# Kernel optimization log

Hardware: AMD Instinct MI355X
Metric: run time of the kernel (lower is better)

Reference implementation:

```python
import jax, jax.numpy as jnp
import numpy as np

B, S, H = 2, 4096, 768
E, R, D = 2, 4, 256          # engines, state_rank, prod(state_mode_sizes)=16*16
FEAT = 6 + 2 * R              # engine_state_feature_dim
IMPRESSION_RATE = 0.05
EPS = 1e-6


def setup_inputs() -> dict:
    key = jax.random.key(0)
    ks = jax.random.split(key, 20)
    n = jax.random.normal
    inv = lambda f: 1.0 / np.sqrt(f)
    return {
        "x": n(ks[0], (B, S, H), jnp.float32),
        # ComplexLinear signal_proj: hidden -> state_dim
        "Wsig_r": n(ks[1], (H, D), jnp.float32) * inv(H),
        "Wsig_i": n(ks[2], (H, D), jnp.float32) * inv(H),
        "bsig_r": jnp.zeros((D,), jnp.float32),
        "bsig_i": jnp.zeros((D,), jnp.float32),
        # per-engine complex recurrence params [E,R,D]
        "log_decay": n(ks[3], (E, R, D), jnp.float32) * 0.5 + 2.0,
        "theta": n(ks[4], (E, R, D), jnp.float32) * 0.1,
        "Bin_r": n(ks[5], (E, R, D), jnp.float32) * inv(D),
        "Bin_i": n(ks[6], (E, R, D), jnp.float32) * inv(D),
        # per-engine ComplexLinear feat -> hidden  [E,FEAT,H]
        "Wsh_r": n(ks[7], (E, FEAT, H), jnp.float32) * inv(FEAT),
        "Wsh_i": n(ks[8], (E, FEAT, H), jnp.float32) * inv(FEAT),
        "bsh_r": jnp.zeros((E, H), jnp.float32),
        "bsh_i": jnp.zeros((E, H), jnp.float32),
        # fusion ComplexLinear: hidden*E -> hidden
        "Wfus_r": n(ks[9], (E * H, H), jnp.float32) * inv(E * H),
        "Wfus_i": n(ks[10], (E * H, H), jnp.float32) * inv(E * H),
        "bfus_r": jnp.zeros((H,), jnp.float32),
        "bfus_i": jnp.zeros((H,), jnp.float32),
        # gate: Linear(hidden*4 -> hidden)
        "Wgate": n(ks[11], (4 * H, H), jnp.float32) * inv(4 * H),
        "bgate": jnp.zeros((H,), jnp.float32),
    }


def _mixer(x, Wsig_r, Wsig_i, bsig_r, bsig_i, log_decay, theta, Bin_r, Bin_i,
           Wsh_r, Wsh_i, bsh_r, bsh_i, Wfus_r, Wfus_i, bfus_r, bfus_i, Wgate, bgate):
    b, s, _ = x.shape
    # complex signal projection (input is real): [b,s,D]
    sr = x @ Wsig_r + bsig_r
    si = x @ Wsig_i + bsig_i
    # input term per engine/rank: u = B * signal  -> [b,s,E,R,D]
    sre = sr[:, :, None, None, :]
    sie = si[:, :, None, None, :]
    ur = Bin_r * sre - Bin_i * sie
    ui = Bin_r * sie + Bin_i * sre
    # complex decay lambda = exp(-softplus(log_decay)) * exp(i*theta)
    mag = jnp.exp(-jax.nn.softplus(log_decay))
    lr = mag * jnp.cos(theta)
    li = mag * jnp.sin(theta)
    ar = jnp.broadcast_to(lr, ur.shape)
    ai = jnp.broadcast_to(li, ur.shape)

    def comb(c1, c2):
        a1r, a1i, b1r, b1i = c1
        a2r, a2i, b2r, b2i = c2
        return (a1r * a2r - a1i * a2i,
                a1r * a2i + a1i * a2r,
                a2r * b1r - a2i * b1i + b2r,
                a2r * b1i + a2i * b1r + b2i)

    # parallel prefix scan of the linear recurrence h_t = lam*h_{t-1} + u_t (time axis=1)
    _, _, hr, hi = jax.lax.associative_scan(comb, (ar, ai, ur, ui), axis=1)

    # rmsnorm over mode dim of complex magnitude
    inv = jax.lax.rsqrt(jnp.mean(hr * hr + hi * hi, axis=-1, keepdims=True) + EPS)
    hr = hr * inv
    hi = hi * inv
    # nonlinear reciprocation-style correction
    hr2 = hr * (1.0 + IMPRESSION_RATE * jnp.tanh(hi))
    hi2 = hi * (1.0 + IMPRESSION_RATE * jnp.tanh(hr))
    hr, hi = hr2, hi2

    # engine state features: FEAT = 6 + 2R complex scalars per (b,s,e)
    f1r, f1i = hr.mean(-1), hi.mean(-1)                        # [b,s,E,R]
    f2r = (hr * hr - hi * hi).mean(-1)
    f2i = (2.0 * hr * hi).mean(-1)
    p = hr * hr + hi * hi
    g1r, g1i = hr.mean((-2, -1)), hi.mean((-2, -1))            # [b,s,E]
    g2r = (hr * hr - hi * hi).mean((-2, -1))
    g2i = (2.0 * hr * hi).mean((-2, -1))
    g3r = p.mean((-2, -1)); g3i = jnp.zeros_like(g3r)
    g4r = jnp.tanh(hr).mean((-2, -1)); g4i = jnp.tanh(hi).mean((-2, -1))
    g5r = jnp.sqrt((hr * hr).mean((-2, -1)) + EPS)
    g5i = jnp.sqrt((hi * hi).mean((-2, -1)) + EPS)
    g6r = (hr * hi).mean((-2, -1)); g6i = jnp.zeros_like(g6r)
    gr = jnp.stack([g1r, g2r, g3r, g4r, g5r, g6r], axis=-1)    # [b,s,E,6]
    gi = jnp.stack([g1i, g2i, g3i, g4i, g5i, g6i], axis=-1)
    fr = jnp.concatenate([f1r, f2r, gr], axis=-1)              # [b,s,E,FEAT]
    fi = jnp.concatenate([f1i, f2i, gi], axis=-1)

    # per-engine complex projection feat -> hidden
    yr = jnp.einsum('bsef,efh->bseh', fr, Wsh_r) - jnp.einsum('bsef,efh->bseh', fi, Wsh_i) + bsh_r
    yi = jnp.einsum('bsef,efh->bseh', fr, Wsh_i) + jnp.einsum('bsef,efh->bseh', fi, Wsh_r) + bsh_i
    yrf = yr.reshape(b, s, -1)
    yif = yi.reshape(b, s, -1)
    # engine fusion ComplexLinear (hidden*E -> hidden)
    fur = yrf @ Wfus_r - yif @ Wfus_i + bfus_r
    fui = yrf @ Wfus_i + yif @ Wfus_r + bfus_i
    # gated residual output
    gate_in = jnp.concatenate([x, fur, fui, fur * jax.nn.silu(fui)], axis=-1)
    gate = jax.nn.sigmoid(gate_in @ Wgate + bgate)
    return x + gate * fur


def reference(x, Wsig_r, Wsig_i, bsig_r, bsig_i, log_decay, theta, Bin_r, Bin_i,
              Wsh_r, Wsh_i, bsh_r, bsh_i, Wfus_r, Wfus_i, bfus_r, bfus_i, Wgate, bgate):
    return _mixer(x, Wsig_r, Wsig_i, bsig_r, bsig_i, log_decay, theta, Bin_r, Bin_i,
                  Wsh_r, Wsh_i, bsh_r, bsh_i, Wfus_r, Wfus_i, bfus_r, bfus_i, Wgate, bgate)
```

## Files before the change

### kernel.cpp

```cpp
#include <hip/hip_runtime.h>
#include <cstdint>
#include <cstddef>

#define B_ 2
#define S_ 4096
#define H_ 768
#define E_ 2
#define R_ 4
#define D_ 256
#define M_ (B_*S_)
#define NC_ 512
#define LC_ (S_/NC_)
#define KGATE 3072
#define KC_ 16
#define HCHUNK (H_/KC_)
#define NF_ 15

typedef __attribute__((ext_vector_type(4))) float f32x4;
typedef __attribute__((ext_vector_type(8))) short short8;

#define GLL(gsrc, ldst) \
  __builtin_amdgcn_global_load_lds((const __attribute__((address_space(1))) void*)(gsrc), \
                                   (__attribute__((address_space(3))) void*)(ldst), 16, 0, 0)

__device__ __forceinline__ unsigned short f2b(float f){
  union { float f; unsigned u; } v; v.f = f;
  unsigned u = v.u;
  return (unsigned short)((u + 0x7fffu + ((u >> 16) & 1u)) >> 16);
}
__device__ __forceinline__ float b2f(unsigned short b){
  union { unsigned u; float f; } v; v.u = ((unsigned)b) << 16;
  return v.f;
}

__device__ __forceinline__ float ftanh(float x){
  float e = __expf(2.f*x);
  return 1.f - 2.f*__builtin_amdgcn_rcpf(e + 1.f);
}
__device__ __forceinline__ float fsigmoid(float x){
  return __builtin_amdgcn_rcpf(1.f + __expf(-x));
}

__device__ __forceinline__ int permK(int r){
  if (r < 768)  return r;
  if (r < 1536) return 768 + 2*(r - 768);
  if (r < 2304) return 769 + 2*(r - 1536);
  return r;
}

__global__ __launch_bounds__(256) void prep_k(
    const float* __restrict__ x, unsigned short* __restrict__ Agate,
    const float* __restrict__ Wsig_r, const float* __restrict__ Wsig_i,
    const float* __restrict__ Wgate,
    unsigned short* __restrict__ WsigT, unsigned short* __restrict__ WgateT,
    const float* __restrict__ Wsh_r, const float* __restrict__ Wsh_i,
    const float* __restrict__ bsh_r, const float* __restrict__ bsh_i,
    const float* __restrict__ Wfus_r, const float* __restrict__ Wfus_i,
    float* __restrict__ Pr, float* __restrict__ Pi)
{
  __shared__ __align__(16) float smem[1440];
  const int bid = blockIdx.x;
  const int tid = threadIdx.x;

  if (bid < 6144){
    int t = bid*256 + tid;
    int base = t*4;
    int m = base / H_, h = base % H_;
    float4 v = *(const float4*)(x + base);
    ushort4 o;
    o.x = f2b(v.x); o.y = f2b(v.y); o.z = f2b(v.z); o.w = f2b(v.w);
    *(ushort4*)(Agate + (size_t)m*KGATE + h) = o;
    return;
  }
  if (bid < 13056){
    int idx = bid - 6144;
    int z = idx / 2304;
    int rem = idx % 2304;
    int bx = rem % 24, by = rem / 24;
    float (*tile)[33] = (float(*)[33])smem;
    const float* in_; unsigned short* out_; int Rr, Cc;
    if (z == 2){ in_ = Wgate; out_ = WgateT; Rr = 3072; Cc = 768; }
    else { in_ = z ? Wsig_i : Wsig_r; out_ = WsigT + (size_t)z*256*768; Rr = 768; Cc = 256; }
    int c0 = bx*32, r0 = by*32;
    if (c0 >= Cc || r0 >= Rr) return;
    int tx = tid & 31, ty = tid >> 5;
    for (int i = ty; i < 32; i += 8){
      int r = r0 + i, c = c0 + tx;
      tile[i][tx] = (r < Rr && c < Cc) ? in_[(size_t)r*Cc + c] : 0.f;
    }
    __syncthreads();
    for (int i = ty; i < 32; i += 8){
      int c = c0 + i, r = r0 + tx;
      if (c < Cc && r < Rr){
        int rd = (z == 2) ? permK(r) : r;
        out_[(size_t)c*Rr + rd] = f2b(tile[tx][i]);
      }
    }
    return;
  }
  {
    int idx = bid - 13056;
    int hc = idx % 3, kc = (idx/3) % KC_, e = idx / (3*KC_);
    float (*wr)[HCHUNK] = (float(*)[HCHUNK])smem;
    float (*wi)[HCHUNK] = (float(*)[HCHUNK])(smem + NF_*HCHUNK);
    int hp = hc*256 + tid;
    int h0 = kc*HCHUNK;
    for (int i = tid; i < NF_*HCHUNK; i += 256){
      int f = i / HCHUNK, hh = i % HCHUNK;
      if (f < 14){
        wr[f][hh] = Wsh_r[(size_t)(e*14 + f)*H_ + h0 + hh];
        wi[f][hh] = Wsh_i[(size_t)(e*14 + f)*H_ + h0 + hh];
      } else {
        wr[f][hh] = bsh_r[(size_t)e*H_ + h0 + hh];
        wi[f][hh] = bsh_i[(size_t)e*H_ + h0 + hh];
      }
    }
    __syncthreads();
    const float* fr = Wfus_r + (size_t)e*H_*H_;
    const float* fi = Wfus_i + (size_t)e*H_*H_;
    float er[NF_], ei[NF_];
    #pragma unroll
    for (int f = 0; f < NF_; ++f){ er[f]=0.f; ei[f]=0.f; }
    for (int hh = 0; hh < HCHUNK; ++hh){
      float p = fr[(size_t)(h0+hh)*H_ + hp];
      float q = fi[(size_t)(h0+hh)*H_ + hp];
      #pragma unroll
      for (int f = 0; f < NF_; ++f){
        float a = wr[f][hh], c = wi[f][hh];
        er[f] += a*p - c*q;
        ei[f] += a*q + c*p;
      }
    }
    #pragma unroll
    for (int f = 0; f < NF_; ++f){
      size_t idxp = ((size_t)(e*KC_ + kc)*NF_ + f)*H_ + hp;
      Pr[idxp] = er[f];
      Pi[idxp] = ei[f];
    }
  }
}

__global__ __launch_bounds__(256) void sig_bft_k(
    const unsigned short* __restrict__ A, const unsigned short* __restrict__ Bt,
    unsigned short* __restrict__ Cout,
    const float* __restrict__ bsig_r, const float* __restrict__ bsig_i,
    const float* __restrict__ Pr, const float* __restrict__ Pi,
    const float* __restrict__ bfus_r, const float* __restrict__ bfus_i,
    unsigned short* __restrict__ Bft)
{
  __shared__ unsigned short As[2][64*64];
  __shared__ unsigned short Bs[2][128*64];
  const int tid = threadIdx.x;
  if (blockIdx.x >= 512){
    int t = (blockIdx.x - 512)*256 + tid;
    int k = t & 63, n = t >> 6;
    int h = n >> 1, c = n & 1;
    float v = 0.f;
    if (k < 56){
      int e = k / 28, fo = k % 28, f = fo % 14;
      bool im = fo >= 14;
      float sr = 0.f, si = 0.f;
      #pragma unroll
      for (int kc = 0; kc < KC_; ++kc){
        size_t idx = ((size_t)(e*KC_ + kc)*NF_ + f)*H_ + h;
        sr += Pr[idx];
        si += Pi[idx];
      }
      v = im ? (c ? sr : -si) : (c ? si : sr);
    } else if (k == 56){
      float s = 0.f;
      #pragma unroll
      for (int e = 0; e < 2; ++e)
        #pragma unroll
        for (int kc = 0; kc < KC_; ++kc){
          size_t idx = ((size_t)(e*KC_ + kc)*NF_ + 14)*H_ + h;
          s += c ? Pi[idx] : Pr[idx];
        }
      v = s + (c ? bfus_i[h] : bfus_r[h]);
    }
    Bft[t] = f2b(v);
    return;
  }
  const int lda = KGATE, Kn = 768, Nn = 512;
  const int fblk = blockIdx.x;
  const int xcd = fblk & 7;
  const int g = fblk >> 3;
  const int n_idx = g % 4;
  const int m_idx = (g / 4)*8 + xcd;
  const int m0 = m_idx * 64;
  const int n0 = n_idx * 128;
  const int lane = tid & 63;
  const int wv = tid >> 6;
  const int wn = wv * 32;
  const int quad = lane >> 4, l16 = lane & 15;

  const int ra = wv*16 + (lane >> 2);
  const int cswA = ((lane & 3) ^ ((ra >> 1) & 3)) * 8;
  const int rb = wv*32 + (lane >> 2);
  const int cswB = ((lane & 3) ^ ((rb >> 1) & 3)) * 8;
  const unsigned short* gA  = A  + (size_t)(m0 + ra)*lda + cswA;
  const unsigned short* gB0 = Bt + (size_t)(n0 + rb)*Kn + cswB;
  const unsigned short* gB1 = Bt + (size_t)(n0 + rb + 16)*Kn + cswB;

  f32x4 acc[4][2];
  #pragma unroll
  for (int i = 0; i < 4; ++i)
    #pragma unroll
    for (int j = 0; j < 2; ++j)
      acc[i][j] = (f32x4){0.f,0.f,0.f,0.f};

  GLL(gA,       &As[0][wv*512]);
  GLL(gA + 32,  &As[0][2048 + wv*512]);
  GLL(gB0,      &Bs[0][wv*1024]);
  GLL(gB1,      &Bs[0][wv*1024 + 512]);
  GLL(gB0 + 32, &Bs[0][4096 + wv*1024]);
  GLL(gB1 + 32, &Bs[0][4096 + wv*1024 + 512]);

  const int nkb = Kn >> 6;
  for (int kb = 0; kb < nkb; ++kb){
    const int cur = kb & 1;
    __syncthreads();
    if (kb + 1 < nkb){
      const int kk = (kb + 1) * 64;
      GLL(gA  + kk,      &As[cur^1][wv*512]);
      GLL(gA  + kk + 32, &As[cur^1][2048 + wv*512]);
      GLL(gB0 + kk,      &Bs[cur^1][wv*1024]);
      GLL(gB1 + kk,      &Bs[cur^1][wv*1024 + 512]);
      GLL(gB0 + kk + 32, &Bs[cur^1][4096 + wv*1024]);
      GLL(gB1 + kk + 32, &Bs[cur^1][4096 + wv*1024 + 512]);
    }
    #pragma unroll
    for (int sub = 0; sub < 2; ++sub){
      const unsigned short* Ab = &As[cur][sub*2048];
      const unsigned short* Bb = &Bs[cur][sub*4096];
      short8 af[4], bf[2];
      #pragma unroll
      for (int i = 0; i < 4; ++i){
        int Ra = i*16 + l16;
        af[i] = *(const short8*)(&Ab[Ra*32 + ((quad ^ ((Ra>>1)&3)))*8]);
      }
      #pragma unroll
      for (int j = 0; j < 2; ++j){
        int Rb = wn + j*16 + l16;
        bf[j] = *(const short8*)(&Bb[Rb*32 + ((quad ^ ((Rb>>1)&3)))*8]);
      }
      #pragma unroll
      for (int i = 0; i < 4; ++i)
        #pragma unroll
        for (int j = 0; j < 2; ++j)
          acc[i][j] = __builtin_amdgcn_mfma_f32_16x16x32_bf16(af[i], bf[j], acc[i][j], 0, 0, 0);
    }
  }

  #pragma unroll
  for (int i = 0; i < 4; ++i){
    #pragma unroll
    for (int j = 0; j < 2; ++j){
      #pragma unroll
      for (int r = 0; r < 4; ++r){
        int row = m0 + i*16 + quad*4 + r;
        int col = n0 + wn + j*16 + l16;
        float v = acc[i][j][r];
        v += (col < 256) ? bsig_r[col] : bsig_i[col - 256];
        Cout[(size_t)row*Nn + col] = f2b(v);
      }
    }
  }
}

__global__ __launch_bounds__(256) void gemm64_gate_k(
    const unsigned short* __restrict__ A, int lda,
    const unsigned short* __restrict__ Bt,
    int Nn, int Kn,
    float* __restrict__ Cout,
    const float* __restrict__ bgate,
    const unsigned short* __restrict__ Ag)
{
  __shared__ unsigned short As[2][64*64];
  __shared__ unsigned short Bs[2][128*64];
  const int tid = threadIdx.x;
  const int fblk = blockIdx.x;
  const int xcd = fblk & 7;
  const int g = fblk >> 3;
  const int n_idx = g % 6;
  const int m_idx = (g / 6)*8 + xcd;
  const int m0 = m_idx * 64;
  const int n0 = n_idx * 128;
  const int lane = tid & 63;
  const int wv = tid >> 6;
  const int wn = wv * 32;
  const int quad = lane >> 4, l16 = lane & 15;

  const int ra = wv*16 + (lane >> 2);
  const int cswA = ((lane & 3) ^ ((ra >> 1) & 3)) * 8;
  const int rb = wv*32 + (lane >> 2);
  const int cswB = ((lane & 3) ^ ((rb >> 1) & 3)) * 8;
  const unsigned short* gA  = A  + (size_t)(m0 + ra)*lda + cswA;
  const unsigned short* gB0 = Bt + (size_t)(n0 + rb)*Kn + cswB;
  const unsigned short* gB1 = Bt + (size_t)(n0 + rb + 16)*Kn + cswB;

  f32x4 acc[4][2];
  #pragma unroll
  for (int i = 0; i < 4; ++i)
    #pragma unroll
    for (int j = 0; j < 2; ++j)
      acc[i][j] = (f32x4){0.f,0.f,0.f,0.f};

  GLL(gA,       &As[0][wv*512]);
  GLL(gA + 32,  &As[0][2048 + wv*512]);
  GLL(gB0,      &Bs[0][wv*1024]);
  GLL(gB1,      &Bs[0][wv*1024 + 512]);
  GLL(gB0 + 32, &Bs[0][4096 + wv*1024]);
  GLL(gB1 + 32, &Bs[0][4096 + wv*1024 + 512]);

  const int nkb = Kn >> 6;
  for (int kb = 0; kb < nkb; ++kb){
    const int cur = kb & 1;
    __syncthreads();
    if (kb + 1 < nkb){
      const int kk = (kb + 1) * 64;
      GLL(gA  + kk,      &As[cur^1][wv*512]);
      GLL(gA  + kk + 32, &As[cur^1][2048 + wv*512]);
      GLL(gB0 + kk,      &Bs[cur^1][wv*1024]);
      GLL(gB1 + kk,      &Bs[cur^1][wv*1024 + 512]);
      GLL(gB0 + kk + 32, &Bs[cur^1][4096 + wv*1024]);
      GLL(gB1 + kk + 32, &Bs[cur^1][4096 + wv*1024 + 512]);
    }
    #pragma unroll
    for (int sub = 0; sub < 2; ++sub){
      const unsigned short* Ab = &As[cur][sub*2048];
      const unsigned short* Bb = &Bs[cur][sub*4096];
      short8 af[4], bf[2];
      #pragma unroll
      for (int i = 0; i < 4; ++i){
        int Ra = i*16 + l16;
        af[i] = *(const short8*)(&Ab[Ra*32 + ((quad ^ ((Ra>>1)&3)))*8]);
      }
      #pragma unroll
      for (int j = 0; j < 2; ++j){
        int Rb = wn + j*16 + l16;
        bf[j] = *(const short8*)(&Bb[Rb*32 + ((quad ^ ((Rb>>1)&3)))*8]);
      }
      #pragma unroll
      for (int i = 0; i < 4; ++i)
        #pragma unroll
        for (int j = 0; j < 2; ++j)
          acc[i][j] = __builtin_amdgcn_mfma_f32_16x16x32_bf16(af[i], bf[j], acc[i][j], 0, 0, 0);
    }
  }

  #pragma unroll
  for (int i = 0; i < 4; ++i){
    #pragma unroll
    for (int j = 0; j < 2; ++j){
      #pragma unroll
      for (int r = 0; r < 4; ++r){
        int row = m0 + i*16 + quad*4 + r;
        int col = n0 + wn + j*16 + l16;
        float v = acc[i][j][r] + bgate[col];
        float gte = fsigmoid(v);
        float xv  = b2f(Ag[(size_t)row*KGATE + col]);
        unsigned fp = *(const unsigned*)(Ag + (size_t)row*KGATE + 768 + 2*col);
        float fur = b2f((unsigned short)(fp & 0xffffu));
        Cout[(size_t)row*768 + col] = xv + gte * fur;
      }
    }
  }
}

__global__ __launch_bounds__(256) void gemm_fg_k(
    const unsigned short* __restrict__ A,
    const unsigned short* __restrict__ Bt,
    unsigned short* __restrict__ Ag)
{
  __shared__ unsigned short As[2*128*32];
  __shared__ unsigned short Bs[2*128*32];
  const int tid = threadIdx.x;
  const int m0 = blockIdx.y * 128;
  const int n0 = blockIdx.x * 128;
  const int lane = tid & 63;
  const int wv = tid >> 6;
  const int wm = (wv >> 1) * 64, wn = (wv & 1) * 64;
  const int quad = lane >> 4, l16 = lane & 15;

  const int srow = wv*32 + (lane >> 2);
  const int csw = ((lane & 3) ^ ((srow >> 1) & 3)) * 8;
  const unsigned short* gA0 = A + (size_t)(m0 + srow)*64 + csw;
  const unsigned short* gA1 = A + (size_t)(m0 + srow + 16)*64 + csw;
  const unsigned short* gB0 = Bt + (size_t)(n0 + srow)*64 + csw;
  const unsigned short* gB1 = Bt + (size_t)(n0 + srow + 16)*64 + csw;

  GLL(gA0,      As + wv*1024);
  GLL(gA1,      As + wv*1024 + 512);
  GLL(gA0 + 32, As + 4096 + wv*1024);
  GLL(gA1 + 32, As + 4096 + wv*1024 + 512);
  GLL(gB0,      Bs + wv*1024);
  GLL(gB1,      Bs + wv*1024 + 512);
  GLL(gB0 + 32, Bs + 4096 + wv*1024);
  GLL(gB1 + 32, Bs + 4096 + wv*1024 + 512);

  f32x4 acc[4][4];
  #pragma unroll
  for (int i = 0; i < 4; ++i)
    #pragma unroll
    for (int j = 0; j < 4; ++j)
      acc[i][j] = (f32x4){0.f,0.f,0.f,0.f};

  __syncthreads();
  #pragma unroll
  for (int kb = 0; kb < 2; ++kb){
    short8 af[4], bf[4];
    #pragma unroll
    for (int i = 0; i < 4; ++i){
      int Ra = wm + i*16 + l16;
      af[i] = *(const short8*)(As + kb*4096 + Ra*32 + ((quad ^ ((Ra>>1)&3)))*8);
    }
    #pragma unroll
    for (int j = 0; j < 4; ++j){
      int Rb = wn + j*16 + l16;
      bf[j] = *(const short8*)(Bs + kb*4096 + Rb*32 + ((quad ^ ((Rb>>1)&3)))*8);
    }
    #pragma unroll
    for (int i = 0; i < 4; ++i)
      #pragma unroll
      for (int j = 0; j < 4; ++j)
        acc[i][j] = __builtin_amdgcn_mfma_f32_16x16x32_bf16(af[i], bf[j], acc[i][j], 0, 0, 0);
  }

  #pragma unroll
  for (int i = 0; i < 4; ++i){
    #pragma unroll
    for (int j = 0; j < 4; ++j){
      #pragma unroll
      for (int r = 0; r < 4; ++r){
        int row = m0 + wm + i*16 + quad*4 + r;
        int col = n0 + wn + j*16 + l16;
        float v = acc[i][j][r];
        float partner = __shfl_xor(v, 1);
        if (!(col & 1)){
          float fur = v, fui = partner;
          unsigned pack = ((unsigned)f2b(fui) << 16) | (unsigned)f2b(fur);
          *(unsigned*)(Ag + (size_t)row*KGATE + 768 + col) = pack;
          float z = fur * fui * fsigmoid(fui);
          Ag[(size_t)row*KGATE + 2304 + (col >> 1)] = f2b(z);
        }
      }
    }
  }
}

__global__ __launch_bounds__(256) void scan_fused_k(
    const unsigned short* __restrict__ S2, const float* __restrict__ log_decay,
    const float* __restrict__ theta, const float* __restrict__ Bin_r,
    const float* __restrict__ Bin_i, float* __restrict__ SPb)
{
  int blk = blockIdx.x;
  int cb  = blk & (NC_/4 - 1);
  int ber = blk >> 7;
  int r = ber & 3, e = (ber >> 2) & 1, b = ber >> 3;
  int wv = threadIdx.x >> 6;
  int c  = cb*4 + wv;
  int lane = threadIdx.x & 63;
  int chan = (e*R_ + r)*D_;
  float lr[4], li[4], br[4], bi[4], hr[4], hi[4];
  {
    float4 ldv = *(const float4*)(log_decay + chan + lane*4);
    float4 thv = *(const float4*)(theta     + chan + lane*4);
    float4 brv = *(const float4*)(Bin_r     + chan + lane*4);
    float4 biv = *(const float4*)(Bin_i     + chan + lane*4);
    const float* ldp = (const float*)&ldv;
    const float* thp = (const float*)&thv;
    const float* brp = (const float*)&brv;
    const float* bip = (const float*)&biv;
    #pragma unroll
    for (int j = 0; j < 4; ++j){
      float ld = ldp[j], th = thp[j];
      float sp = (ld > 20.f) ? ld : log1pf(expf(ld));
      float mag = expf(-sp);
      lr[j] = mag * cosf(th); li[j] = mag * sinf(th);
      br[j] = brp[j]; bi[j] = bip[j];
      hr[j] = 0.f; hi[j] = 0.f;
    }
  }
  if (c > 0){
    size_t wbase = ((size_t)b*S_ + (size_t)(c-1)*LC_) * 512;
    for (int t = 0; t < LC_; ++t){
      const unsigned short* row = S2 + wbase + (size_t)t*512;
      ushort4 vr = *(const ushort4*)(row + lane*4);
      ushort4 vi = *(const ushort4*)(row + 256 + lane*4);
      const unsigned short* pr = (const unsigned short*)&vr;
      const unsigned short* pi = (const unsigned short*)&vi;
      #pragma unroll
      for (int j = 0; j < 4; ++j){
        float sr = b2f(pr[j]), si = b2f(pi[j]);
        float ur = br[j]*sr - bi[j]*si;
        float ui = br[j]*si + bi[j]*sr;
        float nr = lr[j]*hr[j] - li[j]*hi[j] + ur;
        float ni = lr[j]*hi[j] + li[j]*hr[j] + ui;
        hr[j] = nr; hi[j] = ni;
      }
    }
  }
  const int a = lane >> 3;
  size_t sbase = ((size_t)b*S_ + (size_t)c*LC_) * 512;
  for (int t = 0; t < LC_; ++t){
    const unsigned short* row = S2 + sbase + (size_t)t*512;
    ushort4 vr = *(const ushort4*)(row + lane*4);
    ushort4 vi = *(const ushort4*)(row + 256 + lane*4);
    const unsigned short* pr = (const unsigned short*)&vr;
    const unsigned short* pi = (const unsigned short*)&vi;
    #pragma unroll
    for (int j = 0; j < 4; ++j){
      float sr = b2f(pr[j]), si = b2f(pi[j]);
      float ur = br[j]*sr - bi[j]*si;
      float ui = br[j]*si + bi[j]*sr;
      float nr = lr[j]*hr[j] - li[j]*hi[j] + ur;
      float ni = lr[j]*hi[j] + li[j]*hr[j] + ui;
      hr[j] = nr; hi[j] = ni;
    }
    float p = 0.f;
    #pragma unroll
    for (int j = 0; j < 4; ++j) p += hr[j]*hr[j] + hi[j]*hi[j];
    #pragma unroll
    for (int o = 32; o > 0; o >>= 1) p += __shfl_xor(p, o);
    float inv = rsqrtf(p * (1.f/256.f) + 1e-6f);
    float q0=0.f,q1=0.f,q2=0.f,q3=0.f,q4=0.f,q5=0.f,q6=0.f;
    #pragma unroll
    for (int j = 0; j < 4; ++j){
      float xr = hr[j]*inv, xi = hi[j]*inv;
      float thi = ftanh(xi), thr = ftanh(xr);
      float yr = xr * (1.f + 0.05f*thi);
      float yi = xi * (1.f + 0.05f*thr);
      q0 += yr; q1 += yi;
      q2 += yr*yr; q3 += yi*yi; q4 += yr*yi;
      q5 += ftanh(yr); q6 += ftanh(yi);
    }
    #pragma unroll
    for (int o = 32; o >= 8; o >>= 1){
      q0 += __shfl_xor(q0, o); q1 += __shfl_xor(q1, o); q2 += __shfl_xor(q2, o);
      q3 += __shfl_xor(q3, o); q4 += __shfl_xor(q4, o); q5 += __shfl_xor(q5, o);
      q6 += __shfl_xor(q6, o);
    }
    float v = q0;
    v = (a == 1) ? q1 : v;
    v = (a == 2) ? q2 : v;
    v = (a == 3) ? q3 : v;
    v = (a == 4) ? q4 : v;
    v = (a == 5) ? q5 : v;
    v = (a == 6) ? q6 : v;
    v += __shfl_xor(v, 4);
    v += __shfl_xor(v, 2);
    v += __shfl_xor(v, 1);
    if ((lane & 7) == 0 && a < 7){
      int s = c*LC_ + t;
      float* o_ = SPb + ((((size_t)b*S_ + s)*E_ + e)*R_ + r)*7;
      o_[a] = v;
    }
  }
}

__global__ void assemble_feat_k(const float* __restrict__ SPb, unsigned short* __restrict__ featB){
  int t = blockIdx.x*256 + threadIdx.x;
  int e = t & 1, m = t >> 1;
  float shr[4], shi[4], sr2[4], si2[4], srhi[4], str_[4], sti[4];
  #pragma unroll
  for (int r = 0; r < 4; ++r){
    const float* p = SPb + (((size_t)m*E_ + e)*R_ + r)*7;
    shr[r]=p[0]; shi[r]=p[1]; sr2[r]=p[2]; si2[r]=p[3]; srhi[r]=p[4]; str_[r]=p[5]; sti[r]=p[6];
  }
  const float invD = 1.f/256.f, invRD = 1.f/1024.f;
  float fr[14], fi[14];
  float SHr=0,SHi=0,SS2r=0,SS2i=0,SSrhi=0,SStr=0,SSti=0;
  #pragma unroll
  for (int r = 0; r < 4; ++r){
    fr[r] = shr[r]*invD;            fi[r] = shi[r]*invD;
    fr[4+r] = (sr2[r]-si2[r])*invD; fi[4+r] = 2.f*srhi[r]*invD;
    SHr += shr[r]; SHi += shi[r]; SS2r += sr2[r]; SS2i += si2[r];
    SSrhi += srhi[r]; SStr += str_[r]; SSti += sti[r];
  }
  fr[8]  = SHr*invRD;              fi[8]  = SHi*invRD;
  fr[9]  = (SS2r - SS2i)*invRD;    fi[9]  = 2.f*SSrhi*invRD;
  fr[10] = (SS2r + SS2i)*invRD;    fi[10] = 0.f;
  fr[11] = SStr*invRD;             fi[11] = SSti*invRD;
  fr[12] = sqrtf(SS2r*invRD + 1e-6f); fi[12] = sqrtf(SS2i*invRD + 1e-6f);
  fr[13] = SSrhi*invRD;            fi[13] = 0.f;
  unsigned short* o = featB + (size_t)m*64 + e*28;
  #pragma unroll
  for (int f = 0; f < 14; ++f){ o[f] = f2b(fr[f]); o[14+f] = f2b(fi[f]); }
  if (e == 0){
    unsigned short* z = featB + (size_t)m*64 + 56;
    z[0] = f2b(1.0f);
    #pragma unroll
    for (int k = 1; k < 8; ++k) z[k] = 0;
  }
}

extern "C" void kernel_launch(void* const* d_in, const int* in_sizes, int n_in,
                              void* d_out, int out_size, void* d_ws, size_t ws_size,
                              hipStream_t stream)
{
  const float* x         = (const float*)d_in[0];
  const float* Wsig_r    = (const float*)d_in[1];
  const float* Wsig_i    = (const float*)d_in[2];
  const float* bsig_r    = (const float*)d_in[3];
  const float* bsig_i    = (const float*)d_in[4];
  const float* log_decay = (const float*)d_in[5];
  const float* theta     = (const float*)d_in[6];
  const float* Bin_r     = (const float*)d_in[7];
  const float* Bin_i     = (const float*)d_in[8];
  const float* Wsh_r     = (const float*)d_in[9];
  const float* Wsh_i     = (const float*)d_in[10];
  const float* bsh_r     = (const float*)d_in[11];
  const float* bsh_i     = (const float*)d_in[12];
  const float* Wfus_r    = (const float*)d_in[13];
  const float* Wfus_i    = (const float*)d_in[14];
  const float* bfus_r    = (const float*)d_in[15];
  const float* bfus_i    = (const float*)d_in[16];
  const float* Wgate     = (const float*)d_in[17];
  const float* bgate     = (const float*)d_in[18];
  float* out = (float*)d_out;

  char* ws = (char*)d_ws;
  size_t off = 0;
  auto take = [&](size_t bytes) -> char* {
    char* p = ws + off;
    off = (off + bytes + 255) & ~(size_t)255;
    return p;
  };
  unsigned short* Agate  = (unsigned short*)take((size_t)M_*KGATE*2);
  unsigned short* WsigT  = (unsigned short*)take((size_t)512*768*2);
  unsigned short* WgateT = (unsigned short*)take((size_t)768*3072*2);
  unsigned short* S2     = (unsigned short*)take((size_t)M_*512*2);
  float* SPb     = (float*)take((size_t)65536*7*4);
  unsigned short* featB = (unsigned short*)take((size_t)M_*64*2);
  unsigned short* Bft = (unsigned short*)take((size_t)1536*64*2);
  float* Pr      = (float*)take((size_t)2*KC_*NF_*768*4);
  float* Pi      = (float*)take((size_t)2*KC_*NF_*768*4);

  prep_k<<<6144 + 6912 + 96, 256, 0, stream>>>(
      x, Agate, Wsig_r, Wsig_i, Wgate, WsigT, WgateT,
      Wsh_r, Wsh_i, bsh_r, bsh_i, Wfus_r, Wfus_i, Pr, Pi);

  sig_bft_k<<<512 + 384, 256, 0, stream>>>(
      Agate, WsigT, S2, bsig_r, bsig_i, Pr, Pi, bfus_r, bfus_i, Bft);

  scan_fused_k<<<16*(NC_/4), 256, 0, stream>>>(S2, log_decay, theta, Bin_r, Bin_i, SPb);

  assemble_feat_k<<<64, 256, 0, stream>>>(SPb, featB);

  gemm_fg_k<<<dim3(12, 64), 256, 0, stream>>>(featB, Bft, Agate);

  gemm64_gate_k<<<768, 256, 0, stream>>>(Agate, KGATE, WgateT, 768, KGATE, out,
                                         bgate, Agate);
}
```

Baseline: 294.3 us.

## Use 32x32 MFMA with intra-block split-K in gate GEMM

The gate GEMM switches from 16x16x32 to 32x32x16 bf16 MFMA. Each pair of waves now covers a 64x64 output quadrant and takes one half of every 64-wide K tile (split-K), with a shared-memory reduction before the sigmoid/residual epilogue. The K loop is also unrolled by two with fixed double-buffer indices. The aim is fewer LDS fragment reads per MFMA and higher MFMA efficiency, at the cost of an extra LDS reduction pass and more accumulator registers.

```diff
diff --git a/kernel.cpp b/kernel.cpp
--- a/kernel.cpp
+++ b/kernel.cpp
@@ -17,6 +17,7 @@
 #define NF_ 15
 
 typedef __attribute__((ext_vector_type(4))) float f32x4;
+typedef __attribute__((ext_vector_type(16))) float f32x16;
 typedef __attribute__((ext_vector_type(8))) short short8;
 
 #define GLL(gsrc, ldst) \
@@ -288,8 +289,9 @@
   const int n0 = n_idx * 128;
   const int lane = tid & 63;
   const int wv = tid >> 6;
-  const int wn = wv * 32;
-  const int quad = lane >> 4, l16 = lane & 15;
+  const int ch = wv & 1;
+  const int kh = wv >> 1;
+  const int l32 = lane & 31, khi = lane >> 5;
 
   const int ra = wv*16 + (lane >> 2);
   const int cswA = ((lane & 3) ^ ((ra >> 1) & 3)) * 8;
@@ -299,73 +301,81 @@
   const unsigned short* gB0 = Bt + (size_t)(n0 + rb)*Kn + cswB;
   const unsigned short* gB1 = Bt + (size_t)(n0 + rb + 16)*Kn + cswB;
 
-  f32x4 acc[4][2];
-  #pragma unroll
-  for (int i = 0; i < 4; ++i)
-    #pragma unroll
-    for (int j = 0; j < 2; ++j)
-      acc[i][j] = (f32x4){0.f,0.f,0.f,0.f};
-
-  GLL(gA,       &As[0][wv*512]);
-  GLL(gA + 32,  &As[0][2048 + wv*512]);
-  GLL(gB0,      &Bs[0][wv*1024]);
-  GLL(gB1,      &Bs[0][wv*1024 + 512]);
-  GLL(gB0 + 32, &Bs[0][4096 + wv*1024]);
-  GLL(gB1 + 32, &Bs[0][4096 + wv*1024 + 512]);
-
+  f32x16 acc00 = {}, acc01 = {}, acc10 = {}, acc11 = {};
+
+#define STAGE_GATE(kkq, buf) { \
+    const int kk = (kkq) * 64; \
+    GLL(gA  + kk,      &As[buf][wv*512]); \
+    GLL(gA  + kk + 32, &As[buf][2048 + wv*512]); \
+    GLL(gB0 + kk,      &Bs[buf][wv*1024]); \
+    GLL(gB1 + kk,      &Bs[buf][wv*1024 + 512]); \
+    GLL(gB0 + kk + 32, &Bs[buf][4096 + wv*1024]); \
+    GLL(gB1 + kk + 32, &Bs[buf][4096 + wv*1024 + 512]); }
+
+#define COMPUTE_GATE(buf) { \
+    _Pragma("unroll") \
+    for (int t = 0; t < 2; ++t){ \
+      short8 af0, af1, bf0, bf1; \
+      { int row = l32;          int kq = t*2 + khi; \
+        af0 = *(const short8*)(&As[buf][kh*2048 + row*32 + ((kq ^ ((row>>1)&3)))*8]); } \
+      { int row = 32 + l32;     int kq = t*2 + khi; \
+        af1 = *(const short8*)(&As[buf][kh*2048 + row*32 + ((kq ^ ((row>>1)&3)))*8]); } \
+      { int row = ch*64 + l32;  int kq = t*2 + khi; \
+        bf0 = *(const short8*)(&Bs[buf][kh*4096 + row*32 + ((kq ^ ((row>>1)&3)))*8]); } \
+      { int row = ch*64 + 32 + l32; int kq = t*2 + khi; \
+        bf1 = *(const short8*)(&Bs[buf][kh*4096 + row*32 + ((kq ^ ((row>>1)&3)))*8]); } \
+      acc00 = __builtin_amdgcn_mfma_f32_32x32x16_bf16(af0, bf0, acc00, 0, 0, 0); \
+      acc01 = __builtin_amdgcn_mfma_f32_32x32x16_bf16(af0, bf1, acc01, 0, 0, 0); \
+      acc10 = __builtin_amdgcn_mfma_f32_32x32x16_bf16(af1, bf0, acc10, 0, 0, 0); \
+      acc11 = __builtin_amdgcn_mfma_f32_32x32x16_bf16(af1, bf1, acc11, 0, 0, 0); \
+    } }
+
+  STAGE_GATE(0, 0);
   const int nkb = Kn >> 6;
-  for (int kb = 0; kb < nkb; ++kb){
-    const int cur = kb & 1;
+  for (int kb = 0; kb < nkb; kb += 2){
     __syncthreads();
-    if (kb + 1 < nkb){
-      const int kk = (kb + 1) * 64;
-      GLL(gA  + kk,      &As[cur^1][wv*512]);
-      GLL(gA  + kk + 32, &As[cur^1][2048 + wv*512]);
-      GLL(gB0 + kk,      &Bs[cur^1][wv*1024]);
-      GLL(gB1 + kk,      &Bs[cur^1][wv*1024 + 512]);
-      GLL(gB0 + kk + 32, &Bs[cur^1][4096 + wv*1024]);
-      GLL(gB1 + kk + 32, &Bs[cur^1][4096 + wv*1024 + 512]);
-    }
-    #pragma unroll
-    for (int sub = 0; sub < 2; ++sub){
-      const unsigned short* Ab = &As[cur][sub*2048];
-      const unsigned short* Bb = &Bs[cur][sub*4096];
-      short8 af[4], bf[2];
-      #pragma unroll
-      for (int i = 0; i < 4; ++i){
-        int Ra = i*16 + l16;
-        af[i] = *(const short8*)(&Ab[Ra*32 + ((quad ^ ((Ra>>1)&3)))*8]);
-      }
-      #pragma unroll
-      for (int j = 0; j < 2; ++j){
-        int Rb = wn + j*16 + l16;
-        bf[j] = *(const short8*)(&Bb[Rb*32 + ((quad ^ ((Rb>>1)&3)))*8]);
-      }
-      #pragma unroll
-      for (int i = 0; i < 4; ++i)
-        #pragma unroll
-        for (int j = 0; j < 2; ++j)
-          acc[i][j] = __builtin_amdgcn_mfma_f32_16x16x32_bf16(af[i], bf[j], acc[i][j], 0, 0, 0);
-    }
-  }
-
-  #pragma unroll
-  for (int i = 0; i < 4; ++i){
-    #pragma unroll
-    for (int j = 0; j < 2; ++j){
-      #pragma unroll
-      for (int r = 0; r < 4; ++r){
-        int row = m0 + i*16 + quad*4 + r;
-        int col = n0 + wn + j*16 + l16;
-        float v = acc[i][j][r] + bgate[col];
-        float gte = fsigmoid(v);
-        float xv  = b2f(Ag[(size_t)row*KGATE + col]);
-        unsigned fp = *(const unsigned*)(Ag + (size_t)row*KGATE + 768 + 2*col);
-        float fur = b2f((unsigned short)(fp & 0xffffu));
-        Cout[(size_t)row*768 + col] = xv + gte * fur;
-      }
-    }
-  }
+    if (kb + 1 < nkb) STAGE_GATE(kb + 1, 1);
+    COMPUTE_GATE(0);
+    __syncthreads();
+    if (kb + 2 < nkb) STAGE_GATE(kb + 2, 0);
+    COMPUTE_GATE(1);
+  }
+
+  __syncthreads();
+  float* red = (float*)Bs;
+  if (kh == 0){
+    #pragma unroll
+    for (int r = 0; r < 16; ++r) red[ch*4096 + 2*1024 + r*64 + lane] = acc10[r];
+    #pragma unroll
+    for (int r = 0; r < 16; ++r) red[ch*4096 + 3*1024 + r*64 + lane] = acc11[r];
+  } else {
+    #pragma unroll
+    for (int r = 0; r < 16; ++r) red[ch*4096 + 0*1024 + r*64 + lane] = acc00[r];
+    #pragma unroll
+    for (int r = 0; r < 16; ++r) red[ch*4096 + 1*1024 + r*64 + lane] = acc01[r];
+  }
+  __syncthreads();
+  #pragma unroll
+  for (int j = 0; j < 2; ++j){
+    #pragma unroll
+    for (int r = 0; r < 16; ++r){
+      float v;
+      if (kh == 0)
+        v = (j ? acc01[r] : acc00[r]) + red[ch*4096 + (0*2 + j)*1024 + r*64 + lane];
+      else
+        v = (j ? acc11[r] : acc10[r]) + red[ch*4096 + (1*2 + j)*1024 + r*64 + lane];
+      int row = m0 + kh*32 + (r & 3) + 8*(r >> 2) + 4*khi;
+      int col = n0 + ch*64 + j*32 + l32;
+      v += bgate[col];
+      float gte = fsigmoid(v);
+      float xv  = b2f(Ag[(size_t)row*KGATE + col]);
+      unsigned fp = *(const unsigned*)(Ag + (size_t)row*KGATE + 768 + 2*col);
+      float fur = b2f((unsigned short)(fp & 0xffffu));
+      Cout[(size_t)row*768 + col] = xv + gte * fur;
+    }
+  }
+#undef STAGE_GATE
+#undef COMPUTE_GATE
 }
 
 __global__ __launch_bounds__(256) void gemm_fg_k(
```

New measurement: 320.2 us. 1.09x slower.
